# Performance work log

Measured on AMD Instinct MI355X. Metric: run time of the kernel, lower is better.

## Reference

```python
import jax, jax.numpy as jnp
import numpy as np

DIM = 1024

def setup_inputs() -> dict:
    key = jax.random.key(0)
    k1, k2, k3, k4, k5 = jax.random.split(key, 5)
    B, S, D = 32, 2048, DIM
    hidden_state = jax.random.normal(k1, (B, D), dtype=jnp.float32)
    encoder_outputs = jax.random.normal(k2, (B, S, D), dtype=jnp.float32)
    # linear1: (2D -> D) with bias; linear2: (D -> 1) no bias
    W1 = jax.random.normal(k3, (2 * D, D), dtype=jnp.float32) / np.sqrt(2 * D)
    b1 = jnp.zeros((D,), dtype=jnp.float32)
    w2 = jax.random.normal(k4, (D,), dtype=jnp.float32) / np.sqrt(D)
    return {"hidden_state": hidden_state, "encoder_outputs": encoder_outputs,
            "W1": W1, "b1": b1, "w2": w2}

def reference(hidden_state, encoder_outputs, W1, b1, w2):
    B, S, D = encoder_outputs.shape
    # concat(encoder_outputs, broadcast hidden) @ W1 == enc @ W1_enc + hid @ W1_hid
    W1_enc, W1_hid = W1[:D], W1[D:]                      # each [D, D]
    enc_proj = jnp.einsum('bsd,de->bse', encoder_outputs, W1_enc)
    hid_proj = jnp.einsum('bd,de->be', hidden_state, W1_hid)
    h = jnp.tanh(enc_proj + hid_proj[:, None, :] + b1)    # [B, S, D]
    e = jnp.einsum('bsd,d->bs', h, w2)                    # [B, S]
    alpha = jax.nn.softmax(e, axis=1)                     # [B, S]
    context = jnp.einsum('bs,bsd->bd', alpha, encoder_outputs)  # [B, D]
    return context
```

## Files before the change

kernel.cpp:

```cpp
#include <hip/hip_runtime.h>
#include <hip/hip_bf16.h>
#include <cstdint>

typedef __bf16 bf16;
typedef __bf16 bf16x8 __attribute__((ext_vector_type(8)));
typedef float  f32x4  __attribute__((ext_vector_type(4)));

#define N_ENCB   0u
#define N_W1BT   134217728u
#define N_C      136314880u
#define N_E      136445952u
#define N_ALPHA  136707072u
#define N_HIDP   136968192u
#define N_CTXP   138016768u
#define N_TOTAL  140113920ull

#define O_W1BT   0u
#define O_C      2097152u
#define O_E      2228224u
#define O_ALPHA  2490368u
#define O_HIDP   2752512u
#define O_CTXP   3801088u

__global__ void k_convert(const float* __restrict__ in, bf16* __restrict__ out) {
    size_t i = ((size_t)blockIdx.x * 256 + threadIdx.x) * 8;
    const size_t stride = (size_t)2048 * 256 * 8;
    for (; i < 67108864ull; i += stride) {
        f32x4 a = *(const f32x4*)(in + i);
        f32x4 b = *(const f32x4*)(in + i + 4);
        bf16x8 o;
        o[0]=(bf16)a[0]; o[1]=(bf16)a[1]; o[2]=(bf16)a[2]; o[3]=(bf16)a[3];
        o[4]=(bf16)b[0]; o[5]=(bf16)b[1]; o[6]=(bf16)b[2]; o[7]=(bf16)b[3];
        *(bf16x8*)(out + i) = o;
    }
}

__global__ void k_cvec_init(const float* __restrict__ b1, float* __restrict__ cvec) {
    int i = blockIdx.x * 256 + threadIdx.x;
    cvec[i] = b1[i & 1023];
}

__global__ void k_hid_atomic(const float* __restrict__ hid, const float* __restrict__ W1,
                             float* __restrict__ cvec) {
    int e = blockIdx.x * 256 + threadIdx.x;
    int dch = blockIdx.y;
    float acc[32];
#pragma unroll
    for (int b = 0; b < 32; ++b) acc[b] = 0.f;
    int d0 = dch * 32;
#pragma unroll 4
    for (int dd = 0; dd < 32; ++dd) {
        int d = d0 + dd;
        float w = W1[(size_t)(1024 + d) * 1024 + e];
#pragma unroll
        for (int b = 0; b < 32; ++b) acc[b] += hid[b * 1024 + d] * w;
    }
#pragma unroll
    for (int b = 0; b < 32; ++b) atomicAdd(&cvec[b * 1024 + e], acc[b]);
}

__global__ void k_hid_partial(const float* __restrict__ hid, const float* __restrict__ W1,
                              float* __restrict__ hidp) {
    int e = blockIdx.x * 256 + threadIdx.x;
    int dch = blockIdx.y;
    float acc[32];
#pragma unroll
    for (int b = 0; b < 32; ++b) acc[b] = 0.f;
    int d0 = dch * 128;
    for (int dd = 0; dd < 128; ++dd) {
        int d = d0 + dd;
        float w = W1[(size_t)(1024 + d) * 1024 + e];
#pragma unroll
        for (int b = 0; b < 32; ++b) acc[b] += hid[b * 1024 + d] * w;
    }
#pragma unroll
    for (int b = 0; b < 32; ++b) hidp[((size_t)dch * 32 + b) * 1024 + e] = acc[b];
}

__global__ void k_hid_reduce(const float* __restrict__ hidp, const float* __restrict__ b1,
                             float* __restrict__ cvec) {
    int i = blockIdx.x * 256 + threadIdx.x;
    int e = i & 1023;
    float s = b1[e];
#pragma unroll
    for (int dch = 0; dch < 8; ++dch) s += hidp[(size_t)dch * 32768 + i];
    cvec[i] = s;
}

__global__ void k_w1t(const float* __restrict__ W1, bf16* __restrict__ w1bt) {
    __shared__ float tile[32][33];
    int tx = threadIdx.x, ty = threadIdx.y;
    int bx = blockIdx.x, by = blockIdx.y;
#pragma unroll
    for (int i = 0; i < 4; ++i)
        tile[ty + i * 8][tx] = W1[(size_t)(by * 32 + ty + i * 8) * 1024 + bx * 32 + tx];
    __syncthreads();
#pragma unroll
    for (int i = 0; i < 4; ++i)
        w1bt[(size_t)(bx * 32 + ty + i * 8) * 1024 + by * 32 + tx] = (bf16)tile[tx][ty + i * 8];
}

__device__ inline float fast_tanh(float x) {
    float e2 = __expf(2.f * x);
    return 1.f - 2.f / (e2 + 1.f);
}

#define SBAR  __builtin_amdgcn_s_barrier()
#define VMC4  asm volatile("s_waitcnt vmcnt(4)" ::: "memory")
#define PRIO1 __builtin_amdgcn_s_setprio(1)
#define PRIO0 __builtin_amdgcn_s_setprio(0)

template<int D, int MH>
__device__ __forceinline__ void rdA(const char* pA0, const char* pA1, bf16x8 (&bA)[4][2]) {
#pragma unroll
    for (int m = 0; m < 4; ++m) {
        bA[m][0] = *(const bf16x8*)(pA0 + D * 32768 + MH * 8192 + m * 2048);
        bA[m][1] = *(const bf16x8*)(pA1 + D * 32768 + MH * 8192 + m * 2048);
    }
}
template<int D, int N0>
__device__ __forceinline__ void rdB(const char* pB0, const char* pB1, bf16x8 (&bB)[4][2]) {
#pragma unroll
    for (int n = 0; n < 2; ++n) {
        bB[N0 + n][0] = *(const bf16x8*)(pB0 + D * 32768 + (N0 + n) * 2048);
        bB[N0 + n][1] = *(const bf16x8*)(pB1 + D * 32768 + (N0 + n) * 2048);
    }
}
template<int MH, int NH>
__device__ __forceinline__ void mfmaQ(bf16x8 (&bA)[4][2], bf16x8 (&bB)[4][2], f32x4 (&acc)[8][4]) {
#pragma unroll
    for (int kk = 0; kk < 2; ++kk)
#pragma unroll
        for (int m = 0; m < 4; ++m)
#pragma unroll
            for (int n = 0; n < 2; ++n)
                acc[MH * 4 + m][NH * 2 + n] = __builtin_amdgcn_mfma_f32_16x16x32_bf16(
                    bA[m][kk], bB[NH * 2 + n][kk], acc[MH * 4 + m][NH * 2 + n], 0, 0, 0);
}

__global__ __launch_bounds__(512, 1) void k_gemm8(
    const bf16* __restrict__ encb, const bf16* __restrict__ w1bt,
    const float* __restrict__ cvec, const float* __restrict__ w2,
    float* __restrict__ ebuf)
{
    __shared__ __align__(16) char smem[131072];
    const int t = threadIdx.x;
    const int lane = t & 63;
    const int w  = t >> 6;
    const int wr = w >> 2;
    const int wc = w & 3;
    const int l15 = lane & 15, g = (lane >> 4) & 3;

    unsigned bidx = blockIdx.x;
    unsigned swz0 = (bidx & 7u) * 128u + (bidx >> 3);
    const int nt  = swz0 & 3;
    const int mt0 = swz0 >> 2;
    const int n0  = nt * 256;

    const int r6  = t >> 3;
    const int gsl = (t & 7) ^ (r6 & 7);
    const char* srcA    = (const char*)encb + (size_t)(mt0 * 256 + r6) * 2048 + gsl * 16;
    const char* srcA_nx = srcA + (size_t)2048 * 2048;
    const char* srcB    = (const char*)w1bt + (size_t)(n0 + r6) * 2048 + gsl * 16;

#define STAGE_A(SRC, D, H, KT) do { \
    const char* _s = (SRC) + (size_t)(H) * 262144 + (size_t)(KT) * 128; \
    __builtin_amdgcn_global_load_lds((const __attribute__((address_space(1))) unsigned int*)_s, \
        (__attribute__((address_space(3))) unsigned int*)(smem + (D) * 32768 + (H) * 16384 + w * 1024), 16, 0, 0); \
    __builtin_amdgcn_global_load_lds((const __attribute__((address_space(1))) unsigned int*)(_s + 131072), \
        (__attribute__((address_space(3))) unsigned int*)(smem + (D) * 32768 + (H) * 16384 + 8192 + w * 1024), 16, 0, 0); \
} while (0)
#define STAGE_B(D, H, KT) do { \
    const char* _s = srcB + (size_t)(H) * 262144 + (size_t)(KT) * 128; \
    __builtin_amdgcn_global_load_lds((const __attribute__((address_space(1))) unsigned int*)_s, \
        (__attribute__((address_space(3))) unsigned int*)(smem + 65536 + (D) * 32768 + (H) * 16384 + w * 1024), 16, 0, 0); \
    __builtin_amdgcn_global_load_lds((const __attribute__((address_space(1))) unsigned int*)(_s + 131072), \
        (__attribute__((address_space(3))) unsigned int*)(smem + 65536 + (D) * 32768 + (H) * 16384 + 8192 + w * 1024), 16, 0, 0); \
} while (0)

    const int rbA = wr * 128 + l15;
    const int rbB = wc * 64 + l15;
    const int sK0 = (g ^ (l15 & 7)) << 4;
    const int sK1 = sK0 ^ 64;
    const char* pA0 = smem + rbA * 128 + sK0;
    const char* pA1 = smem + rbA * 128 + sK1;
    const char* pB0 = smem + 65536 + rbB * 128 + sK0;
    const char* pB1 = smem + 65536 + rbB * 128 + sK1;

    f32x4 acc[8][4] = {};
    bf16x8 bA[4][2], bB[4][2];

    float wv[4];
    int gcol[4];
#pragma unroll
    for (int n = 0; n < 4; ++n) {
        gcol[n] = n0 + wc * 64 + n * 16 + l15;
        wv[n] = w2[gcol[n]];
    }

    STAGE_A(srcA, 0, 0, 0); STAGE_A(srcA, 0, 1, 0);
    STAGE_B(0, 0, 0); STAGE_B(0, 1, 0);
    STAGE_B(1, 0, 1); STAGE_B(1, 1, 1);
    VMC4; SBAR;

#pragma unroll 1
    for (int j = 0; j < 4; ++j) {
#pragma unroll 1
        for (int i = 0; i < 8; ++i) {
            const int st1 = 2 * i + 1;
            const bool last = (i == 7);
            const int st2 = last ? 0 : 2 * i + 2;
            const int st3 = last ? 1 : 2 * i + 3;
            const char* sA2 = last ? ((j < 3) ? srcA_nx : srcA) : srcA;

            rdA<0, 0>(pA0, pA1, bA);
            rdB<0, 0>(pB0, pB1, bB);
            rdB<0, 2>(pB0, pB1, bB);
            STAGE_A(srcA, 1, 0, st1);
            STAGE_A(srcA, 1, 1, st1);
            PRIO1; mfmaQ<0, 0>(bA, bB, acc); mfmaQ<0, 1>(bA, bB, acc); PRIO0;
            SBAR;

            rdA<0, 1>(pA0, pA1, bA);
            STAGE_B(0, 0, st2);
            STAGE_B(0, 1, st2);
            PRIO1; mfmaQ<1, 0>(bA, bB, acc); mfmaQ<1, 1>(bA, bB, acc); PRIO0;
            VMC4;
            SBAR;

            rdA<1, 0>(pA0, pA1, bA);
            rdB<1, 0>(pB0, pB1, bB);
            rdB<1, 2>(pB0, pB1, bB);
            STAGE_A(sA2, 0, 0, st2);
            STAGE_A(sA2, 0, 1, st2);
            PRIO1; mfmaQ<0, 0>(bA, bB, acc); mfmaQ<0, 1>(bA, bB, acc); PRIO0;
            SBAR;

            rdA<1, 1>(pA0, pA1, bA);
            STAGE_B(1, 0, st3);
            STAGE_B(1, 1, st3);
            PRIO1; mfmaQ<1, 0>(bA, bB, acc); mfmaQ<1, 1>(bA, bB, acc); PRIO0;
            VMC4;
            SBAR;
        }

        const int m0j = (mt0 + 8 * j) * 256;
        const int bj  = m0j >> 11;
        float cv[4];
#pragma unroll
        for (int n = 0; n < 4; ++n) cv[n] = cvec[bj * 1024 + gcol[n]];
#pragma unroll
        for (int m = 0; m < 8; ++m) {
#pragma unroll
            for (int r = 0; r < 4; ++r) {
                float s = 0.f;
#pragma unroll
                for (int n = 0; n < 4; ++n)
                    s += fast_tanh(acc[m][n][r] + cv[n]) * wv[n];
                s += __shfl_xor(s, 1); s += __shfl_xor(s, 2);
                s += __shfl_xor(s, 4); s += __shfl_xor(s, 8);
                if (l15 == 0)
                    atomicAdd(&ebuf[m0j + wr * 128 + m * 16 + g * 4 + r], s);
            }
        }
#pragma unroll
        for (int m = 0; m < 8; ++m)
#pragma unroll
            for (int n = 0; n < 4; ++n)
                acc[m][n] = f32x4{0.f, 0.f, 0.f, 0.f};

        srcA = srcA_nx;
        srcA_nx += (size_t)2048 * 2048;
    }
#undef STAGE_A
#undef STAGE_B
}

__global__ __launch_bounds__(256, 3) void k_gemm_e(
    const float* __restrict__ enc, const bf16* __restrict__ w1bt,
    const float* __restrict__ cvec, const float* __restrict__ w2,
    float* __restrict__ ebuf)
{
    __shared__ __align__(16) unsigned char smem[24 * 1024];
    const int t = threadIdx.x;
    const int lane = t & 63;
    const int w = t >> 6;
    const int wr = w >> 1, wc = w & 1;
    const int l15 = lane & 15, g = lane >> 4;

    unsigned raw = blockIdx.x;
    unsigned swz = (raw & 7u) * 512u + (raw >> 3);
    const int nt = swz & 7, mt = swz >> 3;
    const int m0 = mt * 128, n0 = nt * 128;
    const int b = m0 >> 11;

    int rowA = (t >> 3);
    int slotA = (t & 7) ^ (rowA & 7);
    const char* gA0 = (const char*)enc + (size_t)(m0 + rowA) * 4096 + slotA * 16;
    int rowB = (t >> 2);
    int slotB = (t & 3) ^ ((t >> 3) & 3);
    const char* gB0 = (const char*)w1bt + (size_t)(n0 + rowB) * 2048 + slotB * 16;

    int rowA0 = wr * 64 + l15;
    unsigned offA0 = (unsigned)rowA0 * 128 + ((((2 * g)) ^ (l15 & 7)) << 4);
    int rowB0 = wc * 64 + l15;
    unsigned offB0 = 16384u + (unsigned)rowB0 * 64 + (((g ^ ((l15 >> 1) & 3))) << 4);

    f32x4 acc[4][4] = {};

    for (int kt = 0; kt < 32; ++kt) {
        const char* pa = gA0 + kt * 128;
        const char* pb = gB0 + kt * 64;
#pragma unroll
        for (int c = 0; c < 4; ++c)
            __builtin_amdgcn_global_load_lds(
                (const __attribute__((address_space(1))) unsigned int*)(pa + (size_t)c * 131072),
                (__attribute__((address_space(3))) unsigned int*)(smem + c * 4096 + w * 1024), 16, 0, 0);
#pragma unroll
        for (int c = 0; c < 2; ++c)
            __builtin_amdgcn_global_load_lds(
                (const __attribute__((address_space(1))) unsigned int*)(pb + (size_t)c * 131072),
                (__attribute__((address_space(3))) unsigned int*)(smem + 16384 + c * 4096 + w * 1024), 16, 0, 0);
        __syncthreads();

        bf16x8 af[4], bfr[4];
#pragma unroll
        for (int m = 0; m < 4; ++m) {
            unsigned o0 = offA0 + m * 2048;
            f32x4 lo = *(const f32x4*)(smem + o0);
            f32x4 hi = *(const f32x4*)(smem + (o0 ^ 16u));
            bf16x8 a;
            a[0] = (bf16)lo[0]; a[1] = (bf16)lo[1]; a[2] = (bf16)lo[2]; a[3] = (bf16)lo[3];
            a[4] = (bf16)hi[0]; a[5] = (bf16)hi[1]; a[6] = (bf16)hi[2]; a[7] = (bf16)hi[3];
            af[m] = a;
        }
#pragma unroll
        for (int n = 0; n < 4; ++n)
            bfr[n] = *(const bf16x8*)(smem + (offB0 + n * 1024));
#pragma unroll
        for (int m = 0; m < 4; ++m)
#pragma unroll
            for (int n = 0; n < 4; ++n)
                acc[m][n] = __builtin_amdgcn_mfma_f32_16x16x32_bf16(af[m], bfr[n], acc[m][n], 0, 0, 0);
        __syncthreads();
    }

    float cv[4], wv[4];
#pragma unroll
    for (int n = 0; n < 4; ++n) {
        int gcol = n0 + wc * 64 + n * 16 + l15;
        cv[n] = cvec[b * 1024 + gcol];
        wv[n] = w2[gcol];
    }
#pragma unroll
    for (int m = 0; m < 4; ++m) {
#pragma unroll
        for (int r = 0; r < 4; ++r) {
            float s = 0.f;
#pragma unroll
            for (int n = 0; n < 4; ++n)
                s += fast_tanh(acc[m][n][r] + cv[n]) * wv[n];
            s += __shfl_xor(s, 1); s += __shfl_xor(s, 2);
            s += __shfl_xor(s, 4); s += __shfl_xor(s, 8);
            if (l15 == 0)
                atomicAdd(&ebuf[m0 + wr * 64 + m * 16 + g * 4 + r], s);
        }
    }
}

__global__ void k_softmax(const float* __restrict__ ebuf, float* __restrict__ alpha) {
    int bb = blockIdx.x, t = threadIdx.x;
    __shared__ float red[4], red2[4];
    float v[8];
    float mx = -1e30f;
#pragma unroll
    for (int i = 0; i < 8; ++i) { v[i] = ebuf[bb * 2048 + i * 256 + t]; mx = fmaxf(mx, v[i]); }
    for (int o = 32; o > 0; o >>= 1) mx = fmaxf(mx, __shfl_xor(mx, o));
    if ((t & 63) == 0) red[t >> 6] = mx;
    __syncthreads();
    mx = fmaxf(fmaxf(red[0], red[1]), fmaxf(red[2], red[3]));
    float sum = 0.f;
#pragma unroll
    for (int i = 0; i < 8; ++i) { v[i] = __expf(v[i] - mx); sum += v[i]; }
    for (int o = 32; o > 0; o >>= 1) sum += __shfl_xor(sum, o);
    if ((t & 63) == 0) red2[t >> 6] = sum;
    __syncthreads();
    sum = red2[0] + red2[1] + red2[2] + red2[3];
    float inv = 1.f / sum;
#pragma unroll
    for (int i = 0; i < 8; ++i) alpha[bb * 2048 + i * 256 + t] = v[i] * inv;
}

__global__ void k_ctx_partial_b(const bf16* __restrict__ encb, const float* __restrict__ alpha,
                                float* __restrict__ ctxp) {
    int bid = blockIdx.x;
    int bb = bid >> 4, sc = bid & 15;
    int t = threadIdx.x;
    __shared__ float al[128];
    __shared__ float red[128 * 8];
    if (t < 128) al[t] = alpha[bb * 2048 + sc * 128 + t];
    __syncthreads();
    int d0 = (t & 127) * 8;
    int sp = t >> 7;
    float acc[8] = {};
    const bf16* base = encb + ((size_t)bb * 2048 + sc * 128 + sp) * 1024 + d0;
    for (int s = 0; s < 128; s += 2) {
        bf16x8 v = *(const bf16x8*)(base + (size_t)s * 1024);
        float a = al[s + sp];
#pragma unroll
        for (int k = 0; k < 8; ++k) acc[k] += a * (float)v[k];
    }
    if (sp == 1) {
#pragma unroll
        for (int k = 0; k < 8; ++k) red[(t & 127) * 8 + k] = acc[k];
    }
    __syncthreads();
    if (sp == 0) {
        float* o = ctxp + (size_t)bid * 1024 + d0;
#pragma unroll
        for (int k = 0; k < 8; ++k) o[k] = acc[k] + red[t * 8 + k];
    }
}

__global__ void k_ctx_partial(const float* __restrict__ enc, const float* __restrict__ alpha,
                              float* __restrict__ ctxp) {
    int bid = blockIdx.x;
    int bb = bid >> 4, sc = bid & 15;
    int t = threadIdx.x;
    __shared__ float al[128];
    if (t < 128) al[t] = alpha[bb * 2048 + sc * 128 + t];
    __syncthreads();
    f32x4 acc = {0.f, 0.f, 0.f, 0.f};
    const f32x4* base = (const f32x4*)(enc + ((size_t)bb * 2048 + sc * 128) * 1024) + t;
    for (int s = 0; s < 128; ++s) {
        f32x4 vv = base[(size_t)s * 256];
        acc += vv * al[s];
    }
    *((f32x4*)(ctxp + (size_t)bid * 1024) + t) = acc;
}

__global__ void k_ctx_reduce(const float* __restrict__ ctxp, float* __restrict__ out) {
    int i = blockIdx.x * 256 + threadIdx.x;
    int bb = i >> 10, d = i & 1023;
    float s = 0.f;
#pragma unroll
    for (int sc = 0; sc < 16; ++sc) s += ctxp[((size_t)(bb * 16 + sc)) * 1024 + d];
    out[i] = s;
}

extern "C" void kernel_launch(void* const* d_in, const int* in_sizes, int n_in,
                              void* d_out, int out_size, void* d_ws, size_t ws_size,
                              hipStream_t stream) {
    const float* hid = (const float*)d_in[0];
    const float* enc = (const float*)d_in[1];
    const float* W1  = (const float*)d_in[2];
    const float* b1  = (const float*)d_in[3];
    const float* w2  = (const float*)d_in[4];
    float* out = (float*)d_out;
    char* ws = (char*)d_ws;

    if (ws_size >= N_TOTAL) {
        bf16*  encb  = (bf16*)(ws + N_ENCB);
        bf16*  w1bt  = (bf16*)(ws + N_W1BT);
        float* cvec  = (float*)(ws + N_C);
        float* ebuf  = (float*)(ws + N_E);
        float* alpha = (float*)(ws + N_ALPHA);
        float* ctxp  = (float*)(ws + N_CTXP);

        hipMemsetAsync(ebuf, 0, 65536 * sizeof(float), stream);
        k_convert<<<2048, 256, 0, stream>>>(enc, encb);
        k_w1t<<<dim3(32, 32), dim3(32, 8), 0, stream>>>(W1, w1bt);
        k_cvec_init<<<128, 256, 0, stream>>>(b1, cvec);
        k_hid_atomic<<<dim3(4, 32), 256, 0, stream>>>(hid, W1, cvec);
        k_gemm8<<<256, 512, 0, stream>>>(encb, w1bt, cvec, w2, ebuf);
        k_softmax<<<32, 256, 0, stream>>>(ebuf, alpha);
        k_ctx_partial_b<<<512, 256, 0, stream>>>(encb, alpha, ctxp);
        k_ctx_reduce<<<128, 256, 0, stream>>>(ctxp, out);
    } else {
        bf16*  w1bt  = (bf16*)(ws + O_W1BT);
        float* cvec  = (float*)(ws + O_C);
        float* ebuf  = (float*)(ws + O_E);
        float* alpha = (float*)(ws + O_ALPHA);
        float* hidp  = (float*)(ws + O_HIDP);
        float* ctxp  = (float*)(ws + O_CTXP);

        hipMemsetAsync(ebuf, 0, 65536 * sizeof(float), stream);
        k_hid_partial<<<dim3(4, 8), 256, 0, stream>>>(hid, W1, hidp);
        k_w1t<<<dim3(32, 32), dim3(32, 8), 0, stream>>>(W1, w1bt);
        k_hid_reduce<<<128, 256, 0, stream>>>(hidp, b1, cvec);
        k_gemm_e<<<4096, 256, 0, stream>>>(enc, w1bt, cvec, w2, ebuf);
        k_softmax<<<32, 256, 0, stream>>>(ebuf, alpha);
        k_ctx_partial<<<512, 256, 0, stream>>>(enc, alpha, ctxp);
        k_ctx_reduce<<<128, 256, 0, stream>>>(ctxp, out);
    }
}
```

Measured before the change: 263.6 us.

## Restructure GEMM main loop into eight finer-grained barrier-synchronized MFMA phases

Splits each K-half iteration into eight smaller phases that each read one K-slice of A/B fragments from LDS, issue 16 MFMAs, and interleave global-to-LDS staging loads between them with explicit lgkmcnt/vmcnt waits and barriers. The aim is to interleave LDS reads, async global loads and matrix ops more evenly across the waves, and to cut register pressure by holding a single K-slice of fragments. In exchange it doubles the barrier count and adds lgkmcnt(0) waits that can serialize LDS reads with the MFMAs.

Measured after the change: 267.0 us. About the same (+1.3%).

```diff
diff --git a/kernel.cpp b/kernel.cpp
--- a/kernel.cpp
+++ b/kernel.cpp
@@ -106,36 +106,32 @@
 }
 
 #define SBAR  __builtin_amdgcn_s_barrier()
+#define LGKM0 asm volatile("s_waitcnt lgkmcnt(0)" ::: "memory")
+#define VMC2  asm volatile("s_waitcnt vmcnt(2)" ::: "memory")
 #define VMC4  asm volatile("s_waitcnt vmcnt(4)" ::: "memory")
 #define PRIO1 __builtin_amdgcn_s_setprio(1)
 #define PRIO0 __builtin_amdgcn_s_setprio(0)
 
 template<int D, int MH>
-__device__ __forceinline__ void rdA(const char* pA0, const char* pA1, bf16x8 (&bA)[4][2]) {
-#pragma unroll
-    for (int m = 0; m < 4; ++m) {
-        bA[m][0] = *(const bf16x8*)(pA0 + D * 32768 + MH * 8192 + m * 2048);
-        bA[m][1] = *(const bf16x8*)(pA1 + D * 32768 + MH * 8192 + m * 2048);
-    }
-}
-template<int D, int N0>
-__device__ __forceinline__ void rdB(const char* pB0, const char* pB1, bf16x8 (&bB)[4][2]) {
-#pragma unroll
-    for (int n = 0; n < 2; ++n) {
-        bB[N0 + n][0] = *(const bf16x8*)(pB0 + D * 32768 + (N0 + n) * 2048);
-        bB[N0 + n][1] = *(const bf16x8*)(pB1 + D * 32768 + (N0 + n) * 2048);
-    }
-}
-template<int MH, int NH>
-__device__ __forceinline__ void mfmaQ(bf16x8 (&bA)[4][2], bf16x8 (&bB)[4][2], f32x4 (&acc)[8][4]) {
-#pragma unroll
-    for (int kk = 0; kk < 2; ++kk)
-#pragma unroll
-        for (int m = 0; m < 4; ++m)
-#pragma unroll
-            for (int n = 0; n < 2; ++n)
-                acc[MH * 4 + m][NH * 2 + n] = __builtin_amdgcn_mfma_f32_16x16x32_bf16(
-                    bA[m][kk], bB[NH * 2 + n][kk], acc[MH * 4 + m][NH * 2 + n], 0, 0, 0);
+__device__ __forceinline__ void rdA4(const char* p, bf16x8 (&bA)[4]) {
+#pragma unroll
+    for (int m = 0; m < 4; ++m)
+        bA[m] = *(const bf16x8*)(p + D * 32768 + MH * 8192 + m * 2048);
+}
+template<int D>
+__device__ __forceinline__ void rdB4(const char* p, bf16x8 (&bB)[4]) {
+#pragma unroll
+    for (int n = 0; n < 4; ++n)
+        bB[n] = *(const bf16x8*)(p + D * 32768 + n * 2048);
+}
+template<int MH>
+__device__ __forceinline__ void mfma16(bf16x8 (&bA)[4], bf16x8 (&bB)[4], f32x4 (&acc)[8][4]) {
+#pragma unroll
+    for (int m = 0; m < 4; ++m)
+#pragma unroll
+        for (int n = 0; n < 4; ++n)
+            acc[MH * 4 + m][n] = __builtin_amdgcn_mfma_f32_16x16x32_bf16(
+                bA[m], bB[n], acc[MH * 4 + m][n], 0, 0, 0);
 }
 
 __global__ __launch_bounds__(512, 1) void k_gemm8(
@@ -188,7 +184,7 @@
     const char* pB1 = smem + 65536 + rbB * 128 + sK1;
 
     f32x4 acc[8][4] = {};
-    bf16x8 bA[4][2], bB[4][2];
+    bf16x8 bA[4], bB[4];
 
     float wv[4];
     int gcol[4];
@@ -208,40 +204,33 @@
 #pragma unroll 1
         for (int i = 0; i < 8; ++i) {
             const int st1 = 2 * i + 1;
-            const bool last = (i == 7);
-            const int st2 = last ? 0 : 2 * i + 2;
-            const int st3 = last ? 1 : 2 * i + 3;
-            const char* sA2 = last ? ((j < 3) ? srcA_nx : srcA) : srcA;
-
-            rdA<0, 0>(pA0, pA1, bA);
-            rdB<0, 0>(pB0, pB1, bB);
-            rdB<0, 2>(pB0, pB1, bB);
+            const int st2 = (2 * i + 2) & 15;
+            const int st3 = (2 * i + 3) & 15;
+            const char* sA2 = (i == 7) ? ((j < 3) ? srcA_nx : srcA) : srcA;
+
+            rdA4<0, 0>(pA0, bA); rdB4<0>(pB0, bB);
             STAGE_A(srcA, 1, 0, st1);
+            SBAR; LGKM0; PRIO1; mfma16<0>(bA, bB, acc); PRIO0; SBAR;
+            rdA4<0, 1>(pA0, bA);
             STAGE_A(srcA, 1, 1, st1);
-            PRIO1; mfmaQ<0, 0>(bA, bB, acc); mfmaQ<0, 1>(bA, bB, acc); PRIO0;
-            SBAR;
-
-            rdA<0, 1>(pA0, pA1, bA);
+            SBAR; LGKM0; PRIO1; mfma16<1>(bA, bB, acc); PRIO0; SBAR;
+            rdA4<0, 0>(pA1, bA); rdB4<0>(pB1, bB);
+            SBAR; LGKM0; PRIO1; mfma16<0>(bA, bB, acc); PRIO0; SBAR;
+            rdA4<0, 1>(pA1, bA);
             STAGE_B(0, 0, st2);
+            SBAR; LGKM0; PRIO1; mfma16<1>(bA, bB, acc); PRIO0; VMC2; SBAR;
+            rdA4<1, 0>(pA0, bA); rdB4<1>(pB0, bB);
             STAGE_B(0, 1, st2);
-            PRIO1; mfmaQ<1, 0>(bA, bB, acc); mfmaQ<1, 1>(bA, bB, acc); PRIO0;
-            VMC4;
-            SBAR;
-
-            rdA<1, 0>(pA0, pA1, bA);
-            rdB<1, 0>(pB0, pB1, bB);
-            rdB<1, 2>(pB0, pB1, bB);
+            SBAR; LGKM0; PRIO1; mfma16<0>(bA, bB, acc); PRIO0; SBAR;
+            rdA4<1, 1>(pA0, bA);
             STAGE_A(sA2, 0, 0, st2);
+            SBAR; LGKM0; PRIO1; mfma16<1>(bA, bB, acc); PRIO0; SBAR;
+            rdA4<1, 0>(pA1, bA); rdB4<1>(pB1, bB);
             STAGE_A(sA2, 0, 1, st2);
-            PRIO1; mfmaQ<0, 0>(bA, bB, acc); mfmaQ<0, 1>(bA, bB, acc); PRIO0;
-            SBAR;
-
-            rdA<1, 1>(pA0, pA1, bA);
-            STAGE_B(1, 0, st3);
-            STAGE_B(1, 1, st3);
-            PRIO1; mfmaQ<1, 0>(bA, bB, acc); mfmaQ<1, 1>(bA, bB, acc); PRIO0;
-            VMC4;
-            SBAR;
+            SBAR; LGKM0; PRIO1; mfma16<0>(bA, bB, acc); PRIO0; SBAR;
+            rdA4<1, 1>(pA1, bA);
+            STAGE_B(1, 0, st3); STAGE_B(1, 1, st3);
+            SBAR; LGKM0; PRIO1; mfma16<1>(bA, bB, acc); PRIO0; VMC4; SBAR;
         }
 
         const int m0j = (mt0 + 8 * j) * 256;
```
